# Kernel tuning notes

Measured on AMD Instinct MI355X. Metric: run time of the kernel, lower is better.

The kernel has to match this reference:

```python
import jax, jax.numpy as jnp
import numpy as np

B, S, HID = 2, 2048, 2048
H, KVH, D = 32, 8, 64          # query heads, kv heads, head_dim
G = H // KVH                    # GQA group size (num_key_value_groups)
ROT = 32                        # head_dim * partial_rotary_factor
THETA = 10000.0
NEG = -1e9


def setup_inputs() -> dict:
    key = jax.random.key(0)
    ks = jax.random.split(key, 5)
    hidden_states = jax.random.normal(ks[0], (B, S, HID), jnp.float32) * 0.02
    Wq = jax.random.normal(ks[1], (H * D, HID), jnp.float32) * 0.02
    Wk = jax.random.normal(ks[2], (KVH * D, HID), jnp.float32) * 0.02
    Wv = jax.random.normal(ks[3], (KVH * D, HID), jnp.float32) * 0.02
    Wo = jax.random.normal(ks[4], (HID, H * D), jnp.float32) * 0.02
    # rotary embeddings over the partial rotary dims
    inv_freq = 1.0 / (THETA ** (jnp.arange(0, ROT, 2, dtype=jnp.float32) / ROT))
    freqs = jnp.arange(S, dtype=jnp.float32)[:, None] * inv_freq[None, :]  # [S, ROT/2]
    emb = jnp.concatenate([freqs, freqs], axis=-1)                         # [S, ROT]
    cos = jnp.broadcast_to(jnp.cos(emb)[None], (B, S, ROT)).astype(jnp.float32)
    sin = jnp.broadcast_to(jnp.sin(emb)[None], (B, S, ROT)).astype(jnp.float32)
    # HF-style additive causal mask [1, 1, S, S]
    causal = jnp.tril(jnp.ones((S, S), dtype=bool))
    attention_mask = jnp.where(causal, 0.0, NEG).astype(jnp.float32)[None, None]
    return {"hidden_states": hidden_states, "cos": cos, "sin": sin,
            "attention_mask": attention_mask, "Wq": Wq, "Wk": Wk, "Wv": Wv, "Wo": Wo}


def _rotate_half(x):
    half = x.shape[-1] // 2
    return jnp.concatenate([-x[..., half:], x[..., :half]], axis=-1)


def _apply_partial_rope(x, cos, sin):
    # x: [B, h, S, D]; cos/sin: [B, 1, S, ROT]
    xr, xp = x[..., :ROT], x[..., ROT:]
    xr = xr * cos + _rotate_half(xr) * sin
    return jnp.concatenate([xr, xp], axis=-1)


def reference(hidden_states, cos, sin, attention_mask, Wq, Wk, Wv, Wo):
    bsz, q_len, _ = hidden_states.shape
    q = (hidden_states @ Wq.T).reshape(bsz, q_len, H, D).transpose(0, 2, 1, 3)    # [B,H,S,D]
    k = (hidden_states @ Wk.T).reshape(bsz, q_len, KVH, D).transpose(0, 2, 1, 3)  # [B,KVH,S,D]
    v = (hidden_states @ Wv.T).reshape(bsz, q_len, KVH, D).transpose(0, 2, 1, 3)
    cos_e, sin_e = cos[:, None], sin[:, None]  # unsqueeze_dim=1
    q = _apply_partial_rope(q, cos_e, sin_e)
    k = _apply_partial_rope(k, cos_e, sin_e)
    # GQA: group q heads instead of materializing repeat_kv (same math)
    qg = q.reshape(bsz, KVH, G, q_len, D)
    scores = jnp.einsum('bkgsd,bktd->bkgst', qg, k) / jnp.sqrt(jnp.float32(D))
    scores = scores + attention_mask[:, :, None, :, :q_len]  # [B,KVH,G,S,S]
    attn = jax.nn.softmax(scores.astype(jnp.float32), axis=-1).astype(q.dtype)
    out = jnp.einsum('bkgst,bktd->bkgsd', attn, v)
    out = out.reshape(bsz, H, q_len, D).transpose(0, 2, 1, 3).reshape(bsz, q_len, H * D)
    return out @ Wo.T
```

## Files before the change

kernel.cpp:

```cpp
#include <hip/hip_runtime.h>
#include <hip/hip_bf16.h>

#define BATCH 2
#define SEQ 2048
#define HID 2048
#define NH 32
#define NKVH 8
#define HD 64
#define GQ 4
#define ROT 32

typedef __attribute__((ext_vector_type(8))) short bf16x8;
typedef __attribute__((ext_vector_type(8))) unsigned short u16x8;
typedef __attribute__((ext_vector_type(4))) float f32x4;
typedef unsigned int u32;
typedef unsigned short u16;

#define MFMA_BF16(A, B, C) __builtin_amdgcn_mfma_f32_16x16x32_bf16(A, B, C, 0, 0, 0)

#define QSCALE 0.180336880111120f

__device__ __forceinline__ void gload_lds16(const void* g, void* l) {
    __builtin_amdgcn_global_load_lds(
        (const __attribute__((address_space(1))) unsigned int*)g,
        (__attribute__((address_space(3))) unsigned int*)l, 16, 0, 0);
}

__device__ __forceinline__ u16 f2b(float x) {
    union { __hip_bfloat16 h; u16 u; } cv;
    cv.h = __float2bfloat16(x);
    return cv.u;
}
__device__ __forceinline__ u16 f2br(float x) {
    return (u16)((__builtin_bit_cast(u32, x) + 0x8000u) >> 16);
}
__device__ __forceinline__ u32 pack2r(float lo, float hi) {
    u32 a = __builtin_bit_cast(u32, lo) + 0x8000u;
    u32 b = __builtin_bit_cast(u32, hi) + 0x8000u;
    return __builtin_amdgcn_perm(b, a, 0x07060302u);
}

__global__ __launch_bounds__(256) void cast_all(
    const float* __restrict__ hs, const float* __restrict__ Wq,
    const float* __restrict__ Wk, const float* __restrict__ Wv,
    const float* __restrict__ Wo, u16* __restrict__ d_hs, u16* __restrict__ d_Wq,
    u16* __restrict__ d_Wk, u16* __restrict__ d_Wv, u16* __restrict__ d_Wo) {
    const int bx = blockIdx.x;
    const float* s;
    u16* d;
    int off;
    if (bx < 4096) { s = hs; d = d_hs; off = bx; }
    else if (bx < 6144) { s = Wq; d = d_Wq; off = bx - 4096; }
    else if (bx < 6656) { s = Wk; d = d_Wk; off = bx - 6144; }
    else if (bx < 7168) { s = Wv; d = d_Wv; off = bx - 6656; }
    else { s = Wo; d = d_Wo; off = bx - 7168; }
    const size_t i = (size_t)off * 2048 + threadIdx.x * 8;
    const float4 a = *(const float4*)&s[i];
    const float4 b = *(const float4*)&s[i + 4];
    u16x8 v;
    v[0] = f2b(a.x); v[1] = f2b(a.y); v[2] = f2b(a.z); v[3] = f2b(a.w);
    v[4] = f2b(b.x); v[5] = f2b(b.y); v[6] = f2b(b.z); v[7] = f2b(b.w);
    *(u16x8*)&d[i] = v;
}

__global__ __launch_bounds__(512, 2) void qkv_gemm(
    const u16* __restrict__ A, const u16* __restrict__ Wq,
    const u16* __restrict__ Wk, const u16* __restrict__ Wv,
    u16* __restrict__ Qb, u16* __restrict__ Kb, u16* __restrict__ Vt,
    const float* __restrict__ cosp, const float* __restrict__ sinp) {
    extern __shared__ __align__(16) u16 lds[];
    u16* Asl = lds;
    u16* Wsl = lds + 32768;

    const int bid = blockIdx.x;
    const int wg = (bid & 7) * 24 + (bid >> 3);
    const int mt = wg / 12, nt = wg % 12;
    const int m0 = mt * 256;

    int mode, n0;
    const u16* __restrict__ W;
    if (nt < 8)       { mode = 0; W = Wq; n0 = nt * 256; }
    else if (nt < 10) { mode = 1; W = Wk; n0 = (nt - 8) * 256; }
    else              { mode = 2; W = Wv; n0 = (nt - 10) * 256; }

    const int tid = threadIdx.x;
    const int lane = tid & 63, w = tid >> 6;
    const int wr = w >> 2, wc = w & 3;
    const int ar = lane & 15, quad = lane >> 4, q4 = quad * 4;

    f32x4 acc[8][4] = {};
    bf16x8 af[4][2], wf0[2][2], wf1[2][2];

#define STAGE_A_Q(b, h, c, tt) { \
    const int ci_ = (c) * 512 + tid; \
    const int row_ = ci_ >> 3, kcg_ = (ci_ & 7) ^ (row_ & 7); \
    gload_lds16(&A[(size_t)(m0 + (h) * 128 + row_) * HID + (tt) * 64 + kcg_ * 8], \
                &Asl[((b) * 2 + (h)) * 8192 + ci_ * 8]); }
#define STAGE_W_Q(b, h, c, tt) { \
    const int ci_ = (c) * 512 + tid; \
    const int row_ = ci_ >> 3, kcg_ = (ci_ & 7) ^ (row_ & 7); \
    gload_lds16(&W[(size_t)(n0 + (h) * 128 + row_) * HID + (tt) * 64 + kcg_ * 8], \
                &Wsl[((b) * 2 + (h)) * 8192 + ci_ * 8]); }
#define LDA_F(dst, mj, kh) { \
    const int r_ = (mj) * 16 + ar; \
    dst = *(const bf16x8*)&Asl[(cur * 2 + wr) * 8192 + r_ * 64 + \
                               ((((kh) * 4 + quad) ^ (r_ & 7)) * 8)]; }
#define LDW_F(dst, nj, kh) { \
    const int r_ = (wc & 1) * 64 + (nj) * 16 + ar; \
    dst = *(const bf16x8*)&Wsl[(cur * 2 + (wc >> 1)) * 8192 + r_ * 64 + \
                               ((((kh) * 4 + quad) ^ (r_ & 7)) * 8)]; }
#define MFMA_QUAD(mh, nh, WF) \
    _Pragma("unroll") for (int kh = 0; kh < 2; ++kh) \
    _Pragma("unroll") for (int mi = 0; mi < 4; ++mi) \
    _Pragma("unroll") for (int ni = 0; ni < 2; ++ni) \
        acc[(mh) * 4 + mi][(nh) * 2 + ni] = \
            MFMA_BF16(WF[ni][kh], af[mi][kh], acc[(mh) * 4 + mi][(nh) * 2 + ni]);

    STAGE_A_Q(0, 0, 0, 0); STAGE_A_Q(0, 0, 1, 0);
    STAGE_A_Q(0, 1, 0, 0); STAGE_A_Q(0, 1, 1, 0);
    STAGE_W_Q(0, 0, 0, 0); STAGE_W_Q(0, 0, 1, 0);
    STAGE_W_Q(0, 1, 0, 0); STAGE_W_Q(0, 1, 1, 0);
    STAGE_A_Q(1, 0, 0, 1); STAGE_A_Q(1, 0, 1, 1);
    STAGE_A_Q(1, 1, 0, 1); STAGE_A_Q(1, 1, 1, 1);
    STAGE_W_Q(1, 0, 0, 1); STAGE_W_Q(1, 0, 1, 1);
    STAGE_W_Q(1, 1, 0, 1); STAGE_W_Q(1, 1, 1, 1);
    asm volatile("s_waitcnt vmcnt(8)" ::: "memory");
    __builtin_amdgcn_s_barrier();

#pragma unroll 2
    for (int t = 0; t < 32; ++t) {
        const int cur = t & 1;
        const bool st = (t < 30);
        const int t2 = t + 2;
#pragma unroll
        for (int mi = 0; mi < 4; ++mi) { LDA_F(af[mi][0], mi, 0); LDA_F(af[mi][1], mi, 1); }
#pragma unroll
        for (int ni = 0; ni < 2; ++ni) { LDW_F(wf0[ni][0], ni, 0); LDW_F(wf0[ni][1], ni, 1); }
        __builtin_amdgcn_s_barrier();
        asm volatile("s_waitcnt lgkmcnt(0)" ::: "memory");
        __builtin_amdgcn_s_setprio(1);
        MFMA_QUAD(0, 0, wf0);
        __builtin_amdgcn_s_setprio(0);
        __builtin_amdgcn_s_barrier();
#pragma unroll
        for (int ni = 0; ni < 2; ++ni) { LDW_F(wf1[ni][0], 2 + ni, 0); LDW_F(wf1[ni][1], 2 + ni, 1); }
        if (st) { STAGE_A_Q(cur, 0, 0, t2); STAGE_A_Q(cur, 1, 0, t2); }
        __builtin_amdgcn_s_barrier();
        asm volatile("s_waitcnt lgkmcnt(0)" ::: "memory");
        __builtin_amdgcn_s_setprio(1);
        MFMA_QUAD(0, 1, wf1);
        __builtin_amdgcn_s_setprio(0);
        __builtin_amdgcn_s_barrier();
#pragma unroll
        for (int mi = 0; mi < 4; ++mi) { LDA_F(af[mi][0], 4 + mi, 0); LDA_F(af[mi][1], 4 + mi, 1); }
        if (st) { STAGE_W_Q(cur, 0, 0, t2); STAGE_W_Q(cur, 0, 1, t2); }
        __builtin_amdgcn_s_barrier();
        asm volatile("s_waitcnt lgkmcnt(0)" ::: "memory");
        __builtin_amdgcn_s_setprio(1);
        MFMA_QUAD(1, 1, wf1);
        __builtin_amdgcn_s_setprio(0);
        __builtin_amdgcn_s_barrier();
        if (st) {
            STAGE_A_Q(cur, 0, 1, t2); STAGE_A_Q(cur, 1, 1, t2);
            STAGE_W_Q(cur, 1, 0, t2); STAGE_W_Q(cur, 1, 1, t2);
            asm volatile("s_waitcnt vmcnt(8)" ::: "memory");
        } else {
            asm volatile("s_waitcnt vmcnt(0)" ::: "memory");
        }
        __builtin_amdgcn_s_barrier();
        __builtin_amdgcn_s_setprio(1);
        MFMA_QUAD(1, 0, wf0);
        __builtin_amdgcn_s_setprio(0);
        __builtin_amdgcn_s_barrier();
    }

#undef STAGE_A_Q
#undef STAGE_W_Q
#undef LDA_F
#undef LDW_F
#undef MFMA_QUAD

    if (mode < 2) {
        const float SC = (mode == 0) ? QSCALE : 1.0f;
        u16* __restrict__ C = (mode == 0) ? Qb : Kb;
        const int N = (mode == 0) ? 2048 : 512;
#pragma unroll
        for (int mi = 0; mi < 8; ++mi) {
            const int t = m0 + wr * 128 + mi * 16 + ar;
            const float4 c0 = *(const float4*)&cosp[(size_t)t * ROT + q4];
            const float4 s0 = *(const float4*)&sinp[(size_t)t * ROT + q4];
            const float4 c1 = *(const float4*)&cosp[(size_t)t * ROT + 16 + q4];
            const float4 s1 = *(const float4*)&sinp[(size_t)t * ROT + 16 + q4];
            u16* crow = &C[(size_t)t * N + n0 + wc * 64];
            const f32x4 x0 = acc[mi][0], x1 = acc[mi][1];
            const float cr0[4] = {c0.x, c0.y, c0.z, c0.w};
            const float sr0[4] = {s0.x, s0.y, s0.z, s0.w};
            const float cr1[4] = {c1.x, c1.y, c1.z, c1.w};
            const float sr1[4] = {s1.x, s1.y, s1.z, s1.w};
            float o0[4], o1[4];
#pragma unroll
            for (int r = 0; r < 4; ++r) {
                o0[r] = (x0[r] * cr0[r] - x1[r] * sr0[r]) * SC;
                o1[r] = (x1[r] * cr1[r] + x0[r] * sr1[r]) * SC;
            }
            uint2 v;
            v.x = pack2r(o0[0], o0[1]); v.y = pack2r(o0[2], o0[3]);
            *(uint2*)&crow[q4] = v;
            v.x = pack2r(o1[0], o1[1]); v.y = pack2r(o1[2], o1[3]);
            *(uint2*)&crow[16 + q4] = v;
            v.x = pack2r(acc[mi][2][0] * SC, acc[mi][2][1] * SC);
            v.y = pack2r(acc[mi][2][2] * SC, acc[mi][2][3] * SC);
            *(uint2*)&crow[32 + q4] = v;
            v.x = pack2r(acc[mi][3][0] * SC, acc[mi][3][1] * SC);
            v.y = pack2r(acc[mi][3][2] * SC, acc[mi][3][3] * SC);
            *(uint2*)&crow[48 + q4] = v;
        }
    } else {
        u16* Lt = lds;
        __syncthreads();
#pragma unroll
        for (int mi = 0; mi < 8; ++mi) {
            const int tok = wr * 128 + mi * 16 + ar;
#pragma unroll
            for (int ni = 0; ni < 4; ++ni) {
                const int vc = wc * 64 + ni * 16 + q4;
#pragma unroll
                for (int r = 0; r < 4; ++r) {
                    const int vcol = vc + r;
                    const int ti = tok ^ (((vcol >> 2) & 3) << 4);
                    Lt[vcol * 256 + ti] = f2br(acc[mi][ni][r]);
                }
            }
        }
        __syncthreads();
        for (int it = 0; it < 32; ++it) {
            const int vcol = it * 8 + w;
            const int gcol = n0 + vcol;
            const int kvh = gcol >> 6, d = gcol & 63;
            const int xsw = ((vcol >> 2) & 3) << 4;
            const int s0l = lane * 4;
            const uint2 vv = *(const uint2*)&Lt[vcol * 256 + (s0l ^ xsw)];
            const int g = m0 + s0l;
            const int bb = g >> 11;
            const int s = g & 2047;
            const int ca = (s >> 2) & 7;
            const int cl = ((ca & 3) << 1) | (ca >> 2);
            const int spos = (s & ~31) + cl * 4;
            *(uint2*)&Vt[((size_t)(bb * NKVH + kvh) * HD + d) * SEQ + spos] = vv;
        }
    }
}

__global__ __launch_bounds__(256) void gemm_bt(const u16* __restrict__ A,
                                               const u16* __restrict__ W,
                                               float* __restrict__ C,
                                               int M, int N, int K) {
    const int bid = blockIdx.x;
    const int xcd = bid & 7, loc = bid >> 3;
    const int n0 = (xcd * 2 + (loc & 1)) * 128;
    const int m0 = (loc >> 1) * 128;

    __shared__ __align__(16) u16 As[128 * 64];
    __shared__ __align__(16) u16 Ws[128 * 64];
    const int tid = threadIdx.x;
    const int lane = tid & 63, wave = tid >> 6;
    const int ar = lane & 15, quad = lane >> 4;
    const int q4 = quad * 4;
    const int wm = (wave >> 1) * 64, wn = (wave & 1) * 64;

    f32x4 acc[4][4] = {};

    for (int k0 = 0; k0 < K; k0 += 64) {
#pragma unroll
        for (int it = 0; it < 4; ++it) {
            const int ci = it * 256 + tid;
            const int row = ci >> 3, kcl = ci & 7;
            const int kcg = kcl ^ (row & 7);
            gload_lds16(&A[(size_t)(m0 + row) * K + k0 + kcg * 8], &As[ci * 8]);
            gload_lds16(&W[(size_t)(n0 + row) * K + k0 + kcg * 8], &Ws[ci * 8]);
        }
        __syncthreads();
#pragma unroll
        for (int kh = 0; kh < 2; ++kh) {
            bf16x8 af[4], bf[4];
#pragma unroll
            for (int t = 0; t < 4; ++t) {
                const int ra = wm + t * 16 + ar;
                af[t] = *(const bf16x8*)&As[ra * 64 + (((kh * 4 + quad) ^ (ra & 7))) * 8];
                const int rb = wn + t * 16 + ar;
                bf[t] = *(const bf16x8*)&Ws[rb * 64 + (((kh * 4 + quad) ^ (rb & 7))) * 8];
            }
#pragma unroll
            for (int mt = 0; mt < 4; ++mt)
#pragma unroll
                for (int nt = 0; nt < 4; ++nt)
                    acc[mt][nt] = MFMA_BF16(bf[nt], af[mt], acc[mt][nt]);
        }
        __syncthreads();
    }

#pragma unroll
    for (int mt = 0; mt < 4; ++mt) {
        const int t = m0 + wm + mt * 16 + ar;
#pragma unroll
        for (int nt = 0; nt < 4; ++nt) {
            float4 v = {acc[mt][nt][0], acc[mt][nt][1], acc[mt][nt][2], acc[mt][nt][3]};
            *(float4*)&C[(size_t)t * N + n0 + wn + nt * 16 + q4] = v;
        }
    }
}

__global__ __launch_bounds__(256, 2) void flash_attn_mfma(
    const u16* __restrict__ Qg, const u16* __restrict__ Kg,
    const u16* __restrict__ Vtg, u16* __restrict__ AO) {
    const int p = blockIdx.x, h = blockIdx.y, b = blockIdx.z;
    const int kvh = h / GQ;
    const int tid = threadIdx.x;
    const int lane = tid & 63, w = tid >> 6;
    const int n = lane & 15, quad = lane >> 4;

    __shared__ __align__(16) u16 Qs[128 * 64];
    __shared__ __align__(16) u16 Ks[2 * 64 * 64];
    __shared__ __align__(16) u16 Vts[2 * 64 * 64];

    int rofs[2][4];
#pragma unroll
    for (int j = 0; j < 2; ++j)
#pragma unroll
        for (int t16 = 0; t16 < 4; ++t16) {
            const int row = t16 * 16 + n;
            rofs[j][t16] = row * 64 + (((j * 4 + quad) ^ (row & 7)) * 8);
        }

    const int ci0 = tid, ci1 = 256 + tid;
    const int row0 = ci0 >> 3, kcg0 = (ci0 & 7) ^ (row0 & 7);
    const int row1 = ci1 >> 3, kcg1 = (ci1 & 7) ^ (row1 & 7);
    const u16* kg0 = &Kg[(size_t)((b * SEQ + row0) * NKVH + kvh) * HD + kcg0 * 8];
    const u16* kg1 = &Kg[(size_t)((b * SEQ + row1) * NKVH + kvh) * HD + kcg1 * 8];
    const u16* vg0 = &Vtg[(size_t)((b * NKVH + kvh) * HD + row0) * SEQ + kcg0 * 8];
    const u16* vg1 = &Vtg[(size_t)((b * NKVH + kvh) * HD + row1) * SEQ + kcg1 * 8];
    const f32x4 kZ = {0.f, 0.f, 0.f, 0.f};

    for (int ph = 0; ph < 2; ++ph) {
        const int bq = ph ? (15 - p) : p;
        const int q0 = bq * 128;

#pragma unroll
        for (int it = 0; it < 4; ++it) {
            const int ci = it * 256 + tid;
            const int row = ci >> 3, kcg = (ci & 7) ^ (row & 7);
            gload_lds16(&Qg[(size_t)((b * SEQ + q0 + row) * NH + h) * HD + kcg * 8],
                        &Qs[ci * 8]);
        }
        gload_lds16(kg0, &Ks[ci0 * 8]);
        gload_lds16(kg1, &Ks[ci1 * 8]);
        gload_lds16(vg0, &Vts[ci0 * 8]);
        gload_lds16(vg1, &Vts[ci1 * 8]);
        __syncthreads();

        bf16x8 Qf[2][2];
#pragma unroll
        for (int t = 0; t < 2; ++t)
#pragma unroll
            for (int kh = 0; kh < 2; ++kh) {
                const int qrow = w * 32 + t * 16 + n;
                const int c = (kh * 4 + quad) ^ (qrow & 7);
                Qf[t][kh] = *(const bf16x8*)&Qs[qrow * 64 + c * 8];
            }

        f32x4 O[2][4] = {};
        float lsum[2] = {0.f, 0.f};

        const int ktmax = 2 * bq + 1;
        for (int kt = 0; kt <= ktmax; ++kt) {
            const int cur = kt & 1;
            if (kt < ktmax) {
                const int base = (cur ^ 1) * 4096;
                const size_t ko = (size_t)(kt + 1) * (64 * NKVH * HD);
                const size_t vo = (size_t)(kt + 1) * 64;
                gload_lds16(kg0 + ko, &Ks[base + ci0 * 8]);
                gload_lds16(kg1 + ko, &Ks[base + ci1 * 8]);
                gload_lds16(vg0 + vo, &Vts[base + ci0 * 8]);
                gload_lds16(vg1 + vo, &Vts[base + ci1 * 8]);
            }
            const u16* Kl = &Ks[cur * 4096];
            const u16* Vl = &Vts[cur * 4096];

            f32x4 sc[2][4];
            __builtin_amdgcn_s_setprio(1);
#pragma unroll
            for (int k4 = 0; k4 < 4; ++k4) {
                const bf16x8 Kf0 = *(const bf16x8*)&Kl[rofs[0][k4]];
                sc[0][k4] = MFMA_BF16(Kf0, Qf[0][0], kZ);
                sc[1][k4] = MFMA_BF16(Kf0, Qf[1][0], kZ);
                const bf16x8 Kf1 = *(const bf16x8*)&Kl[rofs[1][k4]];
                sc[0][k4] = MFMA_BF16(Kf1, Qf[0][1], sc[0][k4]);
                sc[1][k4] = MFMA_BF16(Kf1, Qf[1][1], sc[1][k4]);
            }
            __builtin_amdgcn_s_setprio(0);

            const bool masked = (kt >= 2 * bq);
            bf16x8 Pf[2][2];
#pragma unroll
            for (int t = 0; t < 2; ++t) {
                const int qg = q0 + w * 32 + t * 16 + n;
                if (masked) {
#pragma unroll
                    for (int k4 = 0; k4 < 4; ++k4)
#pragma unroll
                        for (int r = 0; r < 4; ++r)
                            if (kt * 64 + k4 * 16 + quad * 4 + r > qg)
                                sc[t][k4][r] = -1e30f;
                }
                float sk[4];
#pragma unroll
                for (int k4 = 0; k4 < 4; ++k4) {
                    const float e0 = __builtin_amdgcn_exp2f(sc[t][k4][0]);
                    const float e1 = __builtin_amdgcn_exp2f(sc[t][k4][1]);
                    const float e2 = __builtin_amdgcn_exp2f(sc[t][k4][2]);
                    const float e3 = __builtin_amdgcn_exp2f(sc[t][k4][3]);
                    sc[t][k4][0] = e0; sc[t][k4][1] = e1;
                    sc[t][k4][2] = e2; sc[t][k4][3] = e3;
                    sk[k4] = (e0 + e1) + (e2 + e3);
                }
                lsum[t] += (sk[0] + sk[1]) + (sk[2] + sk[3]);
#pragma unroll
                for (int kb = 0; kb < 2; ++kb) {
                    union { u32 uw[4]; bf16x8 v; } cv;
#pragma unroll
                    for (int a = 0; a < 2; ++a) {
                        cv.uw[a * 2 + 0] = pack2r(sc[t][2 * kb + a][0], sc[t][2 * kb + a][1]);
                        cv.uw[a * 2 + 1] = pack2r(sc[t][2 * kb + a][2], sc[t][2 * kb + a][3]);
                    }
                    Pf[t][kb] = cv.v;
                }
            }

            __builtin_amdgcn_s_setprio(1);
#pragma unroll
            for (int kb = 0; kb < 2; ++kb)
#pragma unroll
                for (int dt = 0; dt < 4; ++dt) {
                    const bf16x8 Vf = *(const bf16x8*)&Vl[rofs[kb][dt]];
                    O[0][dt] = MFMA_BF16(Vf, Pf[0][kb], O[0][dt]);
                    O[1][dt] = MFMA_BF16(Vf, Pf[1][kb], O[1][dt]);
                }
            __builtin_amdgcn_s_setprio(0);
            __syncthreads();
        }

#pragma unroll
        for (int t = 0; t < 2; ++t) {
            float rs = lsum[t];
            rs += __shfl_xor(rs, 16, 64);
            rs += __shfl_xor(rs, 32, 64);
            const int qg = q0 + w * 32 + t * 16 + n;
            const float inv = 1.f / rs;
#pragma unroll
            for (int dt = 0; dt < 4; ++dt) {
                uint2 v2;
                v2.x = pack2r(O[t][dt][0] * inv, O[t][dt][1] * inv);
                v2.y = pack2r(O[t][dt][2] * inv, O[t][dt][3] * inv);
                *(uint2*)&AO[(size_t)((b * SEQ + qg) * NH + h) * HD + dt * 16 + quad * 4] = v2;
            }
        }
    }
}

extern "C" void kernel_launch(void* const* d_in, const int* in_sizes, int n_in,
                              void* d_out, int out_size, void* d_ws,
                              size_t ws_size, hipStream_t stream) {
    const float* hs = (const float*)d_in[0];
    const float* cosp = (const float*)d_in[1];
    const float* sinp = (const float*)d_in[2];
    const float* Wq = (const float*)d_in[4];
    const float* Wk = (const float*)d_in[5];
    const float* Wv = (const float*)d_in[6];
    const float* Wo = (const float*)d_in[7];
    float* out = (float*)d_out;

    u16* ws = (u16*)d_ws;
    u16* hs_bf = ws;
    u16* Wq_bf = hs_bf + (size_t)4096 * 2048;
    u16* Wk_bf = Wq_bf + (size_t)2048 * 2048;
    u16* Wv_bf = Wk_bf + (size_t)512 * 2048;
    u16* Wo_bf = Wv_bf + (size_t)512 * 2048;
    u16* Qb = Wo_bf + (size_t)2048 * 2048;
    u16* Kb = Qb + (size_t)4096 * 2048;
    u16* Vt = Kb + (size_t)4096 * 512;
    u16* AO = hs_bf;

    static bool attr_done = false;
    if (!attr_done) {
        hipFuncSetAttribute(reinterpret_cast<const void*>(qkv_gemm),
                            hipFuncAttributeMaxDynamicSharedMemorySize, 131072);
        attr_done = true;
    }

    cast_all<<<dim3(9216), 256, 0, stream>>>(hs, Wq, Wk, Wv, Wo, hs_bf, Wq_bf,
                                             Wk_bf, Wv_bf, Wo_bf);

    qkv_gemm<<<dim3(192), 512, 131072, stream>>>(hs_bf, Wq_bf, Wk_bf, Wv_bf,
                                                 Qb, Kb, Vt, cosp, sinp);

    flash_attn_mfma<<<dim3(8, NH, BATCH), 256, 0, stream>>>(Qb, Kb, Vt, AO);

    gemm_bt<<<dim3(512), 256, 0, stream>>>(AO, Wo_bf, out, 4096, 2048, 2048);
}
```

Before: 288.6 us.

## Rewrite output-projection GEMM with 256x128 tiles and double-buffered interleaved pipeline

Replaces the single-buffered 128x128 output-projection GEMM with a 512-thread, 256x128-tile kernel. It double-buffers A and W tiles in dynamic LDS and interleaves global-to-LDS staging with MFMA phases, using explicit waitcnt and barriers. This is meant to hide memory latency and cut the per-k-step full syncs of the old loop. Separately, it drops the s_setprio hints in the flash attention kernel. The added barriers and larger register footprint could limit occupancy.

```diff
diff --git a/kernel.cpp b/kernel.cpp
--- a/kernel.cpp
+++ b/kernel.cpp
@@ -251,61 +251,116 @@
     }
 }
 
-__global__ __launch_bounds__(256) void gemm_bt(const u16* __restrict__ A,
-                                               const u16* __restrict__ W,
-                                               float* __restrict__ C,
-                                               int M, int N, int K) {
+__global__ __launch_bounds__(512, 2) void gemm_bt(const u16* __restrict__ A,
+                                                  const u16* __restrict__ W,
+                                                  float* __restrict__ C,
+                                                  int M, int N, int K) {
+    extern __shared__ __align__(16) u16 lds[];
+    u16* Asl = lds;
+    u16* Wsl = lds + 32768;
+
     const int bid = blockIdx.x;
-    const int xcd = bid & 7, loc = bid >> 3;
-    const int n0 = (xcd * 2 + (loc & 1)) * 128;
-    const int m0 = (loc >> 1) * 128;
-
-    __shared__ __align__(16) u16 As[128 * 64];
-    __shared__ __align__(16) u16 Ws[128 * 64];
+    const int wg = (bid & 7) * 32 + (bid >> 3);
+    const int mt = wg >> 4, nt = wg & 15;
+    const int m0 = mt * 256, n0 = nt * 128;
+
     const int tid = threadIdx.x;
-    const int lane = tid & 63, wave = tid >> 6;
-    const int ar = lane & 15, quad = lane >> 4;
-    const int q4 = quad * 4;
-    const int wm = (wave >> 1) * 64, wn = (wave & 1) * 64;
-
-    f32x4 acc[4][4] = {};
-
-    for (int k0 = 0; k0 < K; k0 += 64) {
-#pragma unroll
-        for (int it = 0; it < 4; ++it) {
-            const int ci = it * 256 + tid;
-            const int row = ci >> 3, kcl = ci & 7;
-            const int kcg = kcl ^ (row & 7);
-            gload_lds16(&A[(size_t)(m0 + row) * K + k0 + kcg * 8], &As[ci * 8]);
-            gload_lds16(&W[(size_t)(n0 + row) * K + k0 + kcg * 8], &Ws[ci * 8]);
-        }
-        __syncthreads();
-#pragma unroll
-        for (int kh = 0; kh < 2; ++kh) {
-            bf16x8 af[4], bf[4];
-#pragma unroll
-            for (int t = 0; t < 4; ++t) {
-                const int ra = wm + t * 16 + ar;
-                af[t] = *(const bf16x8*)&As[ra * 64 + (((kh * 4 + quad) ^ (ra & 7))) * 8];
-                const int rb = wn + t * 16 + ar;
-                bf[t] = *(const bf16x8*)&Ws[rb * 64 + (((kh * 4 + quad) ^ (rb & 7))) * 8];
-            }
-#pragma unroll
-            for (int mt = 0; mt < 4; ++mt)
-#pragma unroll
-                for (int nt = 0; nt < 4; ++nt)
-                    acc[mt][nt] = MFMA_BF16(bf[nt], af[mt], acc[mt][nt]);
-        }
-        __syncthreads();
+    const int lane = tid & 63, w = tid >> 6;
+    const int wr = w >> 2, wc = w & 3;
+    const int ar = lane & 15, quad = lane >> 4, q4 = quad * 4;
+
+    f32x4 acc[8][2] = {};
+    bf16x8 af[4][2], wf0[2], wf1[2];
+
+#define GB_STAGE_A(b, h, c, tt) { \
+    const int ci_ = (c) * 512 + tid; \
+    const int row_ = ci_ >> 3, kcg_ = (ci_ & 7) ^ (row_ & 7); \
+    gload_lds16(&A[(size_t)(m0 + (h) * 128 + row_) * K + (tt) * 64 + kcg_ * 8], \
+                &Asl[((b) * 2 + (h)) * 8192 + ci_ * 8]); }
+#define GB_STAGE_W(b, c, tt) { \
+    const int ci_ = (c) * 512 + tid; \
+    const int row_ = ci_ >> 3, kcg_ = (ci_ & 7) ^ (row_ & 7); \
+    gload_lds16(&W[(size_t)(n0 + row_) * K + (tt) * 64 + kcg_ * 8], \
+                &Wsl[(b) * 8192 + ci_ * 8]); }
+#define GB_LDA(dst, mj, kh) { \
+    const int r_ = (mj) * 16 + ar; \
+    dst = *(const bf16x8*)&Asl[(cur * 2 + wr) * 8192 + r_ * 64 + \
+                               ((((kh) * 4 + quad) ^ (r_ & 7)) * 8)]; }
+#define GB_LDW(dst, nj, kh) { \
+    const int r_ = wc * 32 + (nj) * 16 + ar; \
+    dst = *(const bf16x8*)&Wsl[cur * 8192 + r_ * 64 + \
+                               ((((kh) * 4 + quad) ^ (r_ & 7)) * 8)]; }
+#define GB_MFMA(mh, nj, WF) \
+    _Pragma("unroll") for (int kh = 0; kh < 2; ++kh) \
+    _Pragma("unroll") for (int mi = 0; mi < 4; ++mi) \
+        acc[(mh) * 4 + mi][nj] = MFMA_BF16(WF[kh], af[mi][kh], acc[(mh) * 4 + mi][nj]);
+
+    GB_STAGE_A(0, 0, 0, 0); GB_STAGE_A(0, 1, 0, 0);
+    GB_STAGE_W(0, 0, 0);    GB_STAGE_W(0, 1, 0);
+    GB_STAGE_A(0, 0, 1, 0); GB_STAGE_A(0, 1, 1, 0);
+    GB_STAGE_A(1, 0, 0, 1); GB_STAGE_A(1, 1, 0, 1);
+    GB_STAGE_W(1, 0, 1);    GB_STAGE_W(1, 1, 1);
+    GB_STAGE_A(1, 0, 1, 1); GB_STAGE_A(1, 1, 1, 1);
+    asm volatile("s_waitcnt vmcnt(6)" ::: "memory");
+    __builtin_amdgcn_s_barrier();
+
+#pragma unroll 2
+    for (int t = 0; t < 32; ++t) {
+        const int cur = t & 1;
+        const bool st = (t < 30);
+        const int t2 = t + 2;
+#pragma unroll
+        for (int mi = 0; mi < 4; ++mi) { GB_LDA(af[mi][0], mi, 0); GB_LDA(af[mi][1], mi, 1); }
+        GB_LDW(wf0[0], 0, 0); GB_LDW(wf0[1], 0, 1);
+        __builtin_amdgcn_s_barrier();
+        asm volatile("s_waitcnt lgkmcnt(0)" ::: "memory");
+        __builtin_amdgcn_s_setprio(1);
+        GB_MFMA(0, 0, wf0);
+        __builtin_amdgcn_s_setprio(0);
+        __builtin_amdgcn_s_barrier();
+        GB_LDW(wf1[0], 1, 0); GB_LDW(wf1[1], 1, 1);
+        if (st) { GB_STAGE_A(cur, 0, 0, t2); GB_STAGE_A(cur, 1, 0, t2); }
+        __builtin_amdgcn_s_barrier();
+        asm volatile("s_waitcnt lgkmcnt(0)" ::: "memory");
+        __builtin_amdgcn_s_setprio(1);
+        GB_MFMA(0, 1, wf1);
+        __builtin_amdgcn_s_setprio(0);
+        __builtin_amdgcn_s_barrier();
+#pragma unroll
+        for (int mi = 0; mi < 4; ++mi) { GB_LDA(af[mi][0], 4 + mi, 0); GB_LDA(af[mi][1], 4 + mi, 1); }
+        if (st) { GB_STAGE_W(cur, 0, t2); GB_STAGE_W(cur, 1, t2); }
+        __builtin_amdgcn_s_barrier();
+        asm volatile("s_waitcnt lgkmcnt(0)" ::: "memory");
+        __builtin_amdgcn_s_setprio(1);
+        GB_MFMA(1, 1, wf1);
+        __builtin_amdgcn_s_setprio(0);
+        __builtin_amdgcn_s_barrier();
+        if (st) {
+            GB_STAGE_A(cur, 0, 1, t2); GB_STAGE_A(cur, 1, 1, t2);
+            asm volatile("s_waitcnt vmcnt(6)" ::: "memory");
+        } else {
+            asm volatile("s_waitcnt vmcnt(0)" ::: "memory");
+        }
+        __builtin_amdgcn_s_barrier();
+        __builtin_amdgcn_s_setprio(1);
+        GB_MFMA(1, 0, wf0);
+        __builtin_amdgcn_s_setprio(0);
+        __builtin_amdgcn_s_barrier();
     }
 
-#pragma unroll
-    for (int mt = 0; mt < 4; ++mt) {
-        const int t = m0 + wm + mt * 16 + ar;
-#pragma unroll
-        for (int nt = 0; nt < 4; ++nt) {
-            float4 v = {acc[mt][nt][0], acc[mt][nt][1], acc[mt][nt][2], acc[mt][nt][3]};
-            *(float4*)&C[(size_t)t * N + n0 + wn + nt * 16 + q4] = v;
+#undef GB_STAGE_A
+#undef GB_STAGE_W
+#undef GB_LDA
+#undef GB_LDW
+#undef GB_MFMA
+
+#pragma unroll
+    for (int mi = 0; mi < 8; ++mi) {
+        const int t = m0 + wr * 128 + mi * 16 + ar;
+#pragma unroll
+        for (int ni = 0; ni < 2; ++ni) {
+            float4 v = {acc[mi][ni][0], acc[mi][ni][1], acc[mi][ni][2], acc[mi][ni][3]};
+            *(float4*)&C[(size_t)t * N + n0 + wc * 32 + ni * 16 + q4] = v;
         }
     }
 }
@@ -387,7 +442,6 @@
             const u16* Vl = &Vts[cur * 4096];
 
             f32x4 sc[2][4];
-            __builtin_amdgcn_s_setprio(1);
 #pragma unroll
             for (int k4 = 0; k4 < 4; ++k4) {
                 const bf16x8 Kf0 = *(const bf16x8*)&Kl[rofs[0][k4]];
@@ -397,7 +451,6 @@
                 sc[0][k4] = MFMA_BF16(Kf1, Qf[0][1], sc[0][k4]);
                 sc[1][k4] = MFMA_BF16(Kf1, Qf[1][1], sc[1][k4]);
             }
-            __builtin_amdgcn_s_setprio(0);
 
             const bool masked = (kt >= 2 * bq);
             bf16x8 Pf[2][2];
@@ -436,7 +489,6 @@
                 }
             }
 
-            __builtin_amdgcn_s_setprio(1);
 #pragma unroll
             for (int kb = 0; kb < 2; ++kb)
 #pragma unroll
@@ -445,7 +497,6 @@
                     O[0][dt] = MFMA_BF16(Vf, Pf[0][kb], O[0][dt]);
                     O[1][dt] = MFMA_BF16(Vf, Pf[1][kb], O[1][dt]);
                 }
-            __builtin_amdgcn_s_setprio(0);
             __syncthreads();
         }
 
@@ -494,6 +545,8 @@
     if (!attr_done) {
         hipFuncSetAttribute(reinterpret_cast<const void*>(qkv_gemm),
                             hipFuncAttributeMaxDynamicSharedMemorySize, 131072);
+        hipFuncSetAttribute(reinterpret_cast<const void*>(gemm_bt),
+                            hipFuncAttributeMaxDynamicSharedMemorySize, 98304);
         attr_done = true;
     }
 
@@ -505,5 +558,5 @@
 
     flash_attn_mfma<<<dim3(8, NH, BATCH), 256, 0, stream>>>(Qb, Kb, Vt, AO);
 
-    gemm_bt<<<dim3(512), 256, 0, stream>>>(AO, Wo_bf, out, 4096, 2048, 2048);
-}
+    gemm_bt<<<dim3(256), 512, 98304, stream>>>(AO, Wo_bf, out, 4096, 2048, 2048);
+}
```

Measured after the change: 279.1 us. -3.3%, faster.
